# Performance work log

Hardware: AMD Instinct MI355X
Metric: run time of the kernel (lower is better)

Reference implementation:

```python
import jax, jax.numpy as jnp
import numpy as np

SEQ_LEN, BATCH, HID, EMB, VOCAB = 80, 5120, 256, 8, 100


def lstm_layer(xs, w_ih, w_hh, b_ih, b_hh):
    # xs: [T, B, in]; PyTorch gate order i, f, g, o
    B = xs.shape[1]
    H = w_hh.shape[1]
    x_proj = jnp.einsum('tbi,gi->tbg', xs, w_ih) + b_ih + b_hh  # [T, B, 4H]

    def step(carry, xp_t):
        h, c = carry
        gates = xp_t + h @ w_hh.T
        i, f, g, o = jnp.split(gates, 4, axis=-1)
        c = jax.nn.sigmoid(f) * c + jax.nn.sigmoid(i) * jnp.tanh(g)
        h = jax.nn.sigmoid(o) * jnp.tanh(c)
        return (h, c), h

    init = (jnp.zeros((B, H), xs.dtype), jnp.zeros((B, H), xs.dtype))
    (h_n, c_n), ys = jax.lax.scan(step, init, x_proj)
    return ys, h_n


def setup_inputs() -> dict:
    key = jax.random.key(0)
    ks = jax.random.split(key, 12)
    s_h = 1.0 / np.sqrt(HID)
    inp = {
        'x': jax.random.randint(ks[0], (SEQ_LEN, BATCH), 0, VOCAB),
        'emb': jax.random.normal(ks[1], (VOCAB, EMB), jnp.float32),
        'w_ih0': jax.random.uniform(ks[2], (4 * HID, EMB), jnp.float32, -s_h, s_h),
        'w_hh0': jax.random.uniform(ks[3], (4 * HID, HID), jnp.float32, -s_h, s_h),
        'b_ih0': jax.random.uniform(ks[4], (4 * HID,), jnp.float32, -s_h, s_h),
        'b_hh0': jax.random.uniform(ks[5], (4 * HID,), jnp.float32, -s_h, s_h),
        'w_ih1': jax.random.uniform(ks[6], (4 * HID, HID), jnp.float32, -s_h, s_h),
        'w_hh1': jax.random.uniform(ks[7], (4 * HID, HID), jnp.float32, -s_h, s_h),
        'b_ih1': jax.random.uniform(ks[8], (4 * HID,), jnp.float32, -s_h, s_h),
        'b_hh1': jax.random.uniform(ks[9], (4 * HID,), jnp.float32, -s_h, s_h),
        'dec_w': jax.random.uniform(ks[10], (VOCAB, HID * SEQ_LEN), jnp.float32, -0.01, 0.01),
        'dec_b': jax.random.uniform(ks[11], (VOCAB,), jnp.float32, -0.01, 0.01),
    }
    return inp


def reference(x, emb, w_ih0, w_hh0, b_ih0, b_hh0, w_ih1, w_hh1, b_ih1, b_hh1, dec_w, dec_b):
    encoded = emb[x]                                   # [T, B, EMB]
    ys0, _ = lstm_layer(encoded, w_ih0, w_hh0, b_ih0, b_hh0)  # [T, B, H]
    ys1, _ = lstm_layer(ys0, w_ih1, w_hh1, b_ih1, b_hh1)      # [T, B, H]
    last = ys1[-1]                                     # [B, H] (last timestep)
    # faithful to original quirk: view(-1, hidden*seq_len) -> [B/seq_len, H*T]
    flat = last.reshape(-1, HID * SEQ_LEN)
    return flat @ dec_w.T + dec_b                      # [B/seq_len, VOCAB]
```

## Files before the change

kernel.cpp:

```cpp
#include <hip/hip_runtime.h>

#define T_SEQ 80
#define NB    5120
#define NBH   (NB * 256)
#define NVOC  100

#define OFF_TABLE0 0u
#define OFF_BIAS1  409600u
#define OFF_BPACK  413696u
#define OFF_RING0  1986560u
#define OFF_RING1  7229440u
#define OFF_C0     12472320u
#define OFF_C1     15093760u

#define SMEM_BYTES 63616

typedef float  f32x4  __attribute__((ext_vector_type(4)));
typedef __bf16 bf16x8 __attribute__((ext_vector_type(8)));
typedef short  s16x8  __attribute__((ext_vector_type(8)));
typedef _Float16 f16x4 __attribute__((ext_vector_type(4)));
typedef unsigned short u16x8 __attribute__((ext_vector_type(8)));

__device__ __forceinline__ int colmap(int np) {
  int gate = (np >> 4) & 3;
  int j    = ((np >> 6) << 4) | (np & 15);
  return gate * 256 + j;
}

__device__ __forceinline__ unsigned short f2bf(float f) {
  unsigned int u = __float_as_uint(f);
  u += 0x7fffu + ((u >> 16) & 1u);
  return (unsigned short)(u >> 16);
}
__device__ __forceinline__ float bf2f(unsigned short s) {
  return __uint_as_float(((unsigned int)s) << 16);
}
__device__ __forceinline__ float sigm(float x) {
  x = fminf(fmaxf(x, -20.f), 20.f);
  return 1.f / (1.f + __expf(-x));
}
__device__ __forceinline__ float tanh_(float x) {
  x = fminf(fmaxf(x, -10.f), 10.f);
  float e = __expf(2.f * x);
  return (e - 1.f) / (e + 1.f);
}

__global__ void prep_kernel(const float* __restrict__ emb,
                            const float* __restrict__ w_ih0, const float* __restrict__ w_hh0,
                            const float* __restrict__ b_ih0, const float* __restrict__ b_hh0,
                            const float* __restrict__ w_ih1, const float* __restrict__ w_hh1,
                            const float* __restrict__ b_ih1, const float* __restrict__ b_hh1,
                            float* __restrict__ table0, float* __restrict__ bias1,
                            unsigned short* __restrict__ Bpack) {
  int idx = blockIdx.x * 256 + threadIdx.x;
  if (idx < 102400) {
    int v = idx >> 10, np = idx & 1023;
    int row = colmap(np);
    float s = b_ih0[row] + b_hh0[row];
#pragma unroll
    for (int e = 0; e < 8; ++e) s = fmaf(emb[v * 8 + e], w_ih0[row * 8 + e], s);
    table0[idx] = s;
  } else if (idx < 103424) {
    int np = idx - 102400;
    bias1[np] = b_ih1[colmap(np)] + b_hh1[colmap(np)];
  } else {
    int i2 = idx - 103424;
    int i    = i2 & 7;
    int t    = (i2 >> 3) & 511;
    int ni   = (i2 >> 12) & 7;
    int slot = i2 >> 15;
    int np   = ni * 128 + ((t >> 6) << 4) + (t & 15);
    int row  = colmap(np);
    int k    = (((t & 63) >> 4) << 3) + i;
    float val;
    if (slot < 8) {
      val = w_hh0[row * 256 + slot * 32 + k];
    } else {
      int kc = slot - 8;
      const float* W = (kc < 8) ? w_ih1 : w_hh1;
      val = W[row * 256 + (kc & 7) * 32 + k];
    }
    Bpack[i2] = f2bf(val);
  }
}

__global__ __launch_bounds__(256, 1) void step_kernel(
    int s, const int* __restrict__ x,
    const float* __restrict__ table0, const float* __restrict__ bias1,
    const unsigned short* __restrict__ Bpack,
    unsigned short* __restrict__ ring0, unsigned short* __restrict__ ring1,
    _Float16* __restrict__ c0h, _Float16* __restrict__ c1h) {
  extern __shared__ char smem[];
  char* Ab = smem;
  char* Bb = smem + 38400;
  int*  xs = (int*)(smem + 62976);

  const int tid = threadIdx.x;
  const int lane = tid & 63, wid = tid >> 6;
  const int l15 = lane & 15, lhi = lane >> 4;
  const int wm = wid >> 1, wn = wid & 1, rw = wm * 80;

  const int p = blockIdx.x;
  const int xcd = p & 7, idx = p >> 3;
  const bool isL0 = idx < 32;
  const int sub = idx & 31;
  const int mi = xcd * 4 + (sub >> 3);
  const int ni = sub & 7;
  const int rows = mi * 160;

  int t;
  if (isL0) { if (s == T_SEQ) return; t = s; }
  else      { if (s == 0)     return; t = s - 1; }

  const unsigned short* ring0Prev = ring0 + ((s + 1) & 1) * NBH;
  unsigned short*       ring0Cur  = ring0 + (s & 1) * NBH;
  const unsigned short* h1Prev    = ring1 + (s & 1) * NBH;
  unsigned short*       h1Cur     = ring1 + ((s + 1) & 1) * NBH;

  const int KC = isL0 ? (t > 0 ? 8 : 0) : (t > 0 ? 16 : 8);

  if (isL0 && tid < 160) xs[tid] = x[t * NB + rows + tid];

  f32x4 acc[5][4];
#pragma unroll
  for (int m = 0; m < 5; ++m)
#pragma unroll
    for (int nf = 0; nf < 4; ++nf) acc[m][nf] = (f32x4)0.f;

  uint4 auA0, auA1, auA2, auB0, auB1, auB2;
  s16x8 bsA0, bsA1, bsB0, bsB1;

#define LOADR(S, kc_) do { \
    const unsigned short* _As; int _ko; \
    if (isL0) { _As = ring0Prev; _ko = (kc_) * 32; } \
    else { _As = ((kc_) < 8) ? ring0Prev : h1Prev; _ko = ((kc_) & 7) * 32; } \
    { int _c = tid;       au##S##0 = *(const uint4*)(_As + (rows + (_c >> 2)) * 256 + _ko + ((_c & 3) << 3)); } \
    { int _c = tid + 256; au##S##1 = *(const uint4*)(_As + (rows + (_c >> 2)) * 256 + _ko + ((_c & 3) << 3)); } \
    if (tid < 128) { int _c = tid + 512; au##S##2 = *(const uint4*)(_As + (rows + (_c >> 2)) * 256 + _ko + ((_c & 3) << 3)); } \
    int _slot = isL0 ? (kc_) : (8 + (kc_)); \
    bs##S##0 = *(const s16x8*)(Bpack + (((_slot * 8 + ni) * 512 + tid) << 3)); \
    bs##S##1 = *(const s16x8*)(Bpack + (((_slot * 8 + ni) * 512 + tid + 256) << 3)); \
  } while (0)

#define STORER(S, ob_) do { \
    char* _ab = Ab + (ob_) * 12800; \
    *(uint4*)(_ab + (tid >> 2) * 80 + (tid & 3) * 16) = au##S##0; \
    { int _c = tid + 256; *(uint4*)(_ab + (_c >> 2) * 80 + (_c & 3) * 16) = au##S##1; } \
    if (tid < 128) { int _c = tid + 512; *(uint4*)(_ab + (_c >> 2) * 80 + (_c & 3) * 16) = au##S##2; } \
    char* _bb = Bb + (ob_) * 8192; \
    *(s16x8*)(_bb + tid * 16) = bs##S##0; \
    *(s16x8*)(_bb + (tid + 256) * 16) = bs##S##1; \
  } while (0)

#define CONSUME(ob_) do { \
    const char* _ab = Ab + (ob_) * 12800; \
    const char* _bp = Bb + (ob_) * 8192; \
    bf16x8 _bld[4]; \
    _Pragma("unroll") \
    for (int _nf = 0; _nf < 4; ++_nf) \
      _bld[_nf] = *(const bf16x8*)(_bp + ((wn * 4 + _nf) * 64 + lane) * 16); \
    _Pragma("unroll") \
    for (int _m = 0; _m < 5; ++_m) { \
      bf16x8 _a = *(const bf16x8*)(_ab + (rw + _m * 16 + l15) * 80 + lhi * 16); \
      _Pragma("unroll") \
      for (int _nf = 0; _nf < 4; ++_nf) \
        acc[_m][_nf] = __builtin_amdgcn_mfma_f32_16x16x32_bf16(_a, _bld[_nf], acc[_m][_nf], 0, 0, 0); \
    } \
  } while (0)

  if (KC > 0) {
    LOADR(A, 0);
    LOADR(B, 1);
    STORER(A, 0);
    int bufc = 0;
#pragma unroll 1
    for (int kc = 0; kc < KC; kc += 2) {
      const int b1 = (bufc + 1) % 3, b2 = (bufc + 2) % 3;
      __syncthreads();
      if (kc + 2 < KC) LOADR(A, kc + 2);
      CONSUME(bufc);
      STORER(B, b1);
      __syncthreads();
      if (kc + 3 < KC) LOADR(B, kc + 3);
      CONSUME(b1);
      if (kc + 2 < KC) STORER(A, b2);
      bufc = b2;
    }
  } else {
    __syncthreads();
  }

  const int jh = (ni * 2 + wn) * 16 + l15;
  if (isL0) {
    const int tbb = ni * 128 + wn * 64 + l15;
#pragma unroll
    for (int m = 0; m < 5; ++m) {
      const int cbase = ((rows + rw + m * 16) >> 2) + lhi;
      f16x4 cold4 = (f16x4)(_Float16)0.f;
      if (t > 0) cold4 = *(const f16x4*)(c0h + cbase * 1024 + jh * 4);
      f16x4 cnew;
#pragma unroll
      for (int r = 0; r < 4; ++r) {
        int rowl = rw + m * 16 + lhi * 4 + r;
        const float* tb = table0 + xs[rowl] * 1024 + tbb;
        float gi = acc[m][0][r] + tb[0];
        float gf = acc[m][1][r] + tb[16];
        float gg = acc[m][2][r] + tb[32];
        float go = acc[m][3][r] + tb[48];
        float cn = sigm(gf) * (float)cold4[r] + sigm(gi) * tanh_(gg);
        cnew[r] = (_Float16)cn;
        ring0Cur[(rows + rowl) * 256 + jh] = f2bf(sigm(go) * tanh_(cn));
      }
      *(f16x4*)(c0h + cbase * 1024 + jh * 4) = cnew;
    }
  } else {
    const int bbb = ni * 128 + wn * 64 + l15;
    float b0 = bias1[bbb], b1 = bias1[bbb + 16], b2 = bias1[bbb + 32], b3 = bias1[bbb + 48];
#pragma unroll
    for (int m = 0; m < 5; ++m) {
      const int cbase = ((rows + rw + m * 16) >> 2) + lhi;
      f16x4 cold4 = (f16x4)(_Float16)0.f;
      if (t > 0) cold4 = *(const f16x4*)(c1h + cbase * 1024 + jh * 4);
      f16x4 cnew;
#pragma unroll
      for (int r = 0; r < 4; ++r) {
        int rowl = rw + m * 16 + lhi * 4 + r;
        float gi = acc[m][0][r] + b0;
        float gf = acc[m][1][r] + b1;
        float gg = acc[m][2][r] + b2;
        float go = acc[m][3][r] + b3;
        float cn = sigm(gf) * (float)cold4[r] + sigm(gi) * tanh_(gg);
        cnew[r] = (_Float16)cn;
        h1Cur[(rows + rowl) * 256 + jh] = f2bf(sigm(go) * tanh_(cn));
      }
      *(f16x4*)(c1h + cbase * 1024 + jh * 4) = cnew;
    }
  }
#undef LOADR
#undef STORER
#undef CONSUME
}

__global__ __launch_bounds__(256) void decoder_kernel(
    const unsigned short* __restrict__ h1, const float* __restrict__ dec_w,
    const float* __restrict__ dec_b, float* __restrict__ out) {
  __shared__ float hs[2560];
  const int tid = threadIdx.x, lane = tid & 63, wid = tid >> 6;
  const int b = blockIdx.x;
  const int r = b >> 3;
  const int qoff = (b & 7) * 2560;

  const unsigned short* src = h1 + (size_t)b * 2560;
  for (int i = tid; i < 320; i += 256) {
    u16x8 v8 = *(const u16x8*)(src + i * 8);
#pragma unroll
    for (int e = 0; e < 8; ++e) hs[i * 8 + e] = bf2f(v8[e]);
  }
  __syncthreads();

  for (int vv = wid; vv < NVOC; vv += 4) {
    const float* wp = dec_w + (size_t)vv * 20480 + qoff + lane * 4;
    const float* hp = hs + lane * 4;
    float s = 0.f;
#pragma unroll
    for (int it = 0; it < 10; ++it) {
      f32x4 w4 = *(const f32x4*)(wp + it * 256);
      f32x4 h4 = *(const f32x4*)(hp + it * 256);
      s += w4[0] * h4[0] + w4[1] * h4[1] + w4[2] * h4[2] + w4[3] * h4[3];
    }
#pragma unroll
    for (int off = 32; off > 0; off >>= 1) s += __shfl_down(s, off, 64);
    if (lane == 0) {
      if ((b & 7) == 0) s += dec_b[vv];
      atomicAdd(&out[r * 100 + vv], s);
    }
  }
}

extern "C" void kernel_launch(void* const* d_in, const int* in_sizes, int n_in,
                              void* d_out, int out_size, void* d_ws, size_t ws_size,
                              hipStream_t stream) {
  const int*   x     = (const int*)d_in[0];
  const float* emb   = (const float*)d_in[1];
  const float* w_ih0 = (const float*)d_in[2];
  const float* w_hh0 = (const float*)d_in[3];
  const float* b_ih0 = (const float*)d_in[4];
  const float* b_hh0 = (const float*)d_in[5];
  const float* w_ih1 = (const float*)d_in[6];
  const float* w_hh1 = (const float*)d_in[7];
  const float* b_ih1 = (const float*)d_in[8];
  const float* b_hh1 = (const float*)d_in[9];
  const float* dec_w = (const float*)d_in[10];
  const float* dec_b = (const float*)d_in[11];
  float* out = (float*)d_out;
  char* ws = (char*)d_ws;

  float*          table0 = (float*)(ws + OFF_TABLE0);
  float*          bias1  = (float*)(ws + OFF_BIAS1);
  unsigned short* Bpack  = (unsigned short*)(ws + OFF_BPACK);
  unsigned short* ring0  = (unsigned short*)(ws + OFF_RING0);
  unsigned short* ring1  = (unsigned short*)(ws + OFF_RING1);
  _Float16*       c0h    = (_Float16*)(ws + OFF_C0);
  _Float16*       c1h    = (_Float16*)(ws + OFF_C1);

  hipMemsetAsync(out, 0, (size_t)out_size * 4, stream);
  prep_kernel<<<3476, 256, 0, stream>>>(emb, w_ih0, w_hh0, b_ih0, b_hh0,
                                        w_ih1, w_hh1, b_ih1, b_hh1,
                                        table0, bias1, Bpack);
  hipFuncSetAttribute((const void*)step_kernel,
                      hipFuncAttributeMaxDynamicSharedMemorySize, SMEM_BYTES);
  for (int s = 0; s <= T_SEQ; ++s)
    step_kernel<<<512, 256, SMEM_BYTES, stream>>>(s, x, table0, bias1, Bpack,
                                                  ring0, ring1, c0h, c1h);
  decoder_kernel<<<512, 256, 0, stream>>>(ring1 + NBH, dec_w, dec_b, out);
}
```

Before: 1.648 ms.

## Load MFMA operands directly from global memory into registers, drop LDS staging

Replaces the LDS-staged, barrier-synchronised triple-buffered GEMM pipeline in the per-step LSTM kernel with direct global-to-register loads of A and B fragments in MFMA layout. A three-slot register ring prefetches two K-chunks ahead, and the loops are fully unrolled per layer case. Without shared memory the launch bounds allow two blocks per CU. The aim is to remove LDS round-trips and __syncthreads, at the cost of less coalesced global loads, heavy register pressure, and token ids re-read from global memory in the epilogue.

```diff
diff --git a/kernel.cpp b/kernel.cpp
--- a/kernel.cpp
+++ b/kernel.cpp
@@ -13,11 +13,8 @@
 #define OFF_C0     12472320u
 #define OFF_C1     15093760u
 
-#define SMEM_BYTES 63616
-
 typedef float  f32x4  __attribute__((ext_vector_type(4)));
 typedef __bf16 bf16x8 __attribute__((ext_vector_type(8)));
-typedef short  s16x8  __attribute__((ext_vector_type(8)));
 typedef _Float16 f16x4 __attribute__((ext_vector_type(4)));
 typedef unsigned short u16x8 __attribute__((ext_vector_type(8)));
 
@@ -84,17 +81,12 @@
   }
 }
 
-__global__ __launch_bounds__(256, 1) void step_kernel(
+__global__ __launch_bounds__(256, 2) void step_kernel(
     int s, const int* __restrict__ x,
     const float* __restrict__ table0, const float* __restrict__ bias1,
     const unsigned short* __restrict__ Bpack,
     unsigned short* __restrict__ ring0, unsigned short* __restrict__ ring1,
     _Float16* __restrict__ c0h, _Float16* __restrict__ c1h) {
-  extern __shared__ char smem[];
-  char* Ab = smem;
-  char* Bb = smem + 38400;
-  int*  xs = (int*)(smem + 62976);
-
   const int tid = threadIdx.x;
   const int lane = tid & 63, wid = tid >> 6;
   const int l15 = lane & 15, lhi = lane >> 4;
@@ -117,9 +109,11 @@
   const unsigned short* h1Prev    = ring1 + (s & 1) * NBH;
   unsigned short*       h1Cur     = ring1 + ((s + 1) & 1) * NBH;
 
-  const int KC = isL0 ? (t > 0 ? 8 : 0) : (t > 0 ? 16 : 8);
-
-  if (isL0 && tid < 160) xs[tid] = x[t * NB + rows + tid];
+  const int slotBase = isL0 ? 0 : 8;
+
+  const unsigned short* apR = ring0Prev + (size_t)(rows + rw + l15) * 256 + lhi * 8;
+  const unsigned short* apH = h1Prev    + (size_t)(rows + rw + l15) * 256 + lhi * 8;
+  const unsigned short* bp  = Bpack + ((size_t)(slotBase * 8 + ni) * 512 + wn * 256 + lane) * 8;
 
   f32x4 acc[5][4];
 #pragma unroll
@@ -127,67 +121,53 @@
 #pragma unroll
     for (int nf = 0; nf < 4; ++nf) acc[m][nf] = (f32x4)0.f;
 
-  uint4 auA0, auA1, auA2, auB0, auB1, auB2;
-  s16x8 bsA0, bsA1, bsB0, bsB1;
-
-#define LOADR(S, kc_) do { \
-    const unsigned short* _As; int _ko; \
-    if (isL0) { _As = ring0Prev; _ko = (kc_) * 32; } \
-    else { _As = ((kc_) < 8) ? ring0Prev : h1Prev; _ko = ((kc_) & 7) * 32; } \
-    { int _c = tid;       au##S##0 = *(const uint4*)(_As + (rows + (_c >> 2)) * 256 + _ko + ((_c & 3) << 3)); } \
-    { int _c = tid + 256; au##S##1 = *(const uint4*)(_As + (rows + (_c >> 2)) * 256 + _ko + ((_c & 3) << 3)); } \
-    if (tid < 128) { int _c = tid + 512; au##S##2 = *(const uint4*)(_As + (rows + (_c >> 2)) * 256 + _ko + ((_c & 3) << 3)); } \
-    int _slot = isL0 ? (kc_) : (8 + (kc_)); \
-    bs##S##0 = *(const s16x8*)(Bpack + (((_slot * 8 + ni) * 512 + tid) << 3)); \
-    bs##S##1 = *(const s16x8*)(Bpack + (((_slot * 8 + ni) * 512 + tid + 256) << 3)); \
-  } while (0)
-
-#define STORER(S, ob_) do { \
-    char* _ab = Ab + (ob_) * 12800; \
-    *(uint4*)(_ab + (tid >> 2) * 80 + (tid & 3) * 16) = au##S##0; \
-    { int _c = tid + 256; *(uint4*)(_ab + (_c >> 2) * 80 + (_c & 3) * 16) = au##S##1; } \
-    if (tid < 128) { int _c = tid + 512; *(uint4*)(_ab + (_c >> 2) * 80 + (_c & 3) * 16) = au##S##2; } \
-    char* _bb = Bb + (ob_) * 8192; \
-    *(s16x8*)(_bb + tid * 16) = bs##S##0; \
-    *(s16x8*)(_bb + (tid + 256) * 16) = bs##S##1; \
-  } while (0)
-
-#define CONSUME(ob_) do { \
-    const char* _ab = Ab + (ob_) * 12800; \
-    const char* _bp = Bb + (ob_) * 8192; \
-    bf16x8 _bld[4]; \
+  bf16x8 Ar[3][5], Br[3][4];
+
+#define LOADG(sl_, kc_) do { \
+    const unsigned short* _Ab = (isL0 || (kc_) < 8) ? apR : apH; \
+    const int _ko = ((kc_) & 7) * 32; \
+    _Pragma("unroll") \
+    for (int _m = 0; _m < 5; ++_m) \
+      Ar[sl_][_m] = *(const bf16x8*)(_Ab + _m * 4096 + _ko); \
+    const unsigned short* _Bb = bp + (size_t)(kc_) * 32768; \
     _Pragma("unroll") \
     for (int _nf = 0; _nf < 4; ++_nf) \
-      _bld[_nf] = *(const bf16x8*)(_bp + ((wn * 4 + _nf) * 64 + lane) * 16); \
+      Br[sl_][_nf] = *(const bf16x8*)(_Bb + _nf * 512); \
+  } while (0)
+
+#define MFMAG(sl_) do { \
     _Pragma("unroll") \
-    for (int _m = 0; _m < 5; ++_m) { \
-      bf16x8 _a = *(const bf16x8*)(_ab + (rw + _m * 16 + l15) * 80 + lhi * 16); \
+    for (int _nf = 0; _nf < 4; ++_nf) \
       _Pragma("unroll") \
-      for (int _nf = 0; _nf < 4; ++_nf) \
-        acc[_m][_nf] = __builtin_amdgcn_mfma_f32_16x16x32_bf16(_a, _bld[_nf], acc[_m][_nf], 0, 0, 0); \
-    } \
+      for (int _m = 0; _m < 5; ++_m) \
+        acc[_m][_nf] = __builtin_amdgcn_mfma_f32_16x16x32_bf16(Ar[sl_][_m], Br[sl_][_nf], acc[_m][_nf], 0, 0, 0); \
   } while (0)
 
-  if (KC > 0) {
-    LOADR(A, 0);
-    LOADR(B, 1);
-    STORER(A, 0);
-    int bufc = 0;
-#pragma unroll 1
-    for (int kc = 0; kc < KC; kc += 2) {
-      const int b1 = (bufc + 1) % 3, b2 = (bufc + 2) % 3;
-      __syncthreads();
-      if (kc + 2 < KC) LOADR(A, kc + 2);
-      CONSUME(bufc);
-      STORER(B, b1);
-      __syncthreads();
-      if (kc + 3 < KC) LOADR(B, kc + 3);
-      CONSUME(b1);
-      if (kc + 2 < KC) STORER(A, b2);
-      bufc = b2;
+  if (isL0) {
+    if (t > 0) {
+      LOADG(0, 0); LOADG(1, 1);
+#pragma unroll
+      for (int kc = 0; kc < 8; ++kc) {
+        if (kc + 2 < 8) LOADG((kc + 2) % 3, kc + 2);
+        MFMAG(kc % 3);
+      }
     }
   } else {
-    __syncthreads();
+    if (t > 0) {
+      LOADG(0, 0); LOADG(1, 1);
+#pragma unroll
+      for (int kc = 0; kc < 16; ++kc) {
+        if (kc + 2 < 16) LOADG((kc + 2) % 3, kc + 2);
+        MFMAG(kc % 3);
+      }
+    } else {
+      LOADG(0, 0); LOADG(1, 1);
+#pragma unroll
+      for (int kc = 0; kc < 8; ++kc) {
+        if (kc + 2 < 8) LOADG((kc + 2) % 3, kc + 2);
+        MFMAG(kc % 3);
+      }
+    }
   }
 
   const int jh = (ni * 2 + wn) * 16 + l15;
@@ -202,7 +182,8 @@
 #pragma unroll
       for (int r = 0; r < 4; ++r) {
         int rowl = rw + m * 16 + lhi * 4 + r;
-        const float* tb = table0 + xs[rowl] * 1024 + tbb;
+        int v = x[t * NB + rows + rowl];
+        const float* tb = table0 + v * 1024 + tbb;
         float gi = acc[m][0][r] + tb[0];
         float gf = acc[m][1][r] + tb[16];
         float gg = acc[m][2][r] + tb[32];
@@ -236,9 +217,8 @@
       *(f16x4*)(c1h + cbase * 1024 + jh * 4) = cnew;
     }
   }
-#undef LOADR
-#undef STORER
-#undef CONSUME
+#undef LOADG
+#undef MFMAG
 }
 
 __global__ __launch_bounds__(256) void decoder_kernel(
@@ -307,10 +287,8 @@
   prep_kernel<<<3476, 256, 0, stream>>>(emb, w_ih0, w_hh0, b_ih0, b_hh0,
                                         w_ih1, w_hh1, b_ih1, b_hh1,
                                         table0, bias1, Bpack);
-  hipFuncSetAttribute((const void*)step_kernel,
-                      hipFuncAttributeMaxDynamicSharedMemorySize, SMEM_BYTES);
   for (int s = 0; s <= T_SEQ; ++s)
-    step_kernel<<<512, 256, SMEM_BYTES, stream>>>(s, x, table0, bias1, Bpack,
-                                                  ring0, ring1, c0h, c1h);
+    step_kernel<<<512, 256, 0, stream>>>(s, x, table0, bias1, Bpack,
+                                         ring0, ring1, c0h, c1h);
   decoder_kernel<<<512, 256, 0, stream>>>(ring1 + NBH, dec_w, dec_b, out);
 }
```

Measured after the change: 2.242 ms. 1.36x slower.
